# Kernel tuning notes

Measured on AMD Instinct MI355X. Metric: run time of the kernel, lower is better.

Reference implementation:

```python
import jax, jax.numpy as jnp
import numpy as np

C = 1.0            # PoincareBall curvature
BALL_EPS = 4e-3    # geoopt projx eps for float32
MIN_NORM = 1e-15


def artanh(x):
    x = jnp.clip(x, -1.0 + 1e-7, 1.0 - 1e-7)
    return 0.5 * (jnp.log1p(x) - jnp.log1p(-x))


def project(x):
    # geoopt projx: clip norm to (1 - eps) / sqrt(c)
    norm = jnp.maximum(jnp.linalg.norm(x, axis=-1, keepdims=True), MIN_NORM)
    maxnorm = (1.0 - BALL_EPS) / jnp.sqrt(C)
    return jnp.where(norm > maxnorm, x / norm * maxnorm, x)


def mobius_matvec(M, x):
    # geoopt mobius_matvec on PoincareBall (followed by project)
    sqrt_c = jnp.sqrt(C)
    x_norm = jnp.maximum(jnp.linalg.norm(x, axis=-1, keepdims=True), MIN_NORM)
    mx = x @ M.T
    mx_norm = jnp.maximum(jnp.linalg.norm(mx, axis=-1, keepdims=True), MIN_NORM)
    res = jnp.tanh(mx_norm / x_norm * artanh(sqrt_c * x_norm)) * mx / (mx_norm * sqrt_c)
    zero_mx = jnp.all(mx == 0.0, axis=-1, keepdims=True)
    return project(jnp.where(zero_mx, 0.0, res))


def mobius_add(x, y):
    # geoopt mobius_add on PoincareBall (followed by project)
    x2 = jnp.sum(x * x, axis=-1, keepdims=True)
    y2 = jnp.sum(y * y, axis=-1, keepdims=True)
    xy = jnp.sum(x * y, axis=-1, keepdims=True)
    num = (1.0 + 2.0 * C * xy + C * y2) * x + (1.0 - C * x2) * y
    den = jnp.maximum(1.0 + 2.0 * C * xy + C * C * x2 * y2, MIN_NORM)
    return project(num / den)


def hyp_linear(x, W, b):
    out = mobius_matvec(W, x)
    return mobius_add(out, b)


def hyperbolic_scores(q, k):
    # q, k: [B, H, S, Dh]
    eps = 1e-5
    q_norm_sq = jnp.minimum(jnp.sum(q * q, axis=-1, keepdims=True), 1.0 - eps)  # [B,H,S,1]
    k_norm_sq = jnp.minimum(jnp.sum(k * k, axis=-1, keepdims=True), 1.0 - eps)  # [B,H,S,1]
    qk = jnp.einsum('bhqd,bhkd->bhqk', q, k)
    k_norm_sq_t = jnp.swapaxes(k_norm_sq, -2, -1)                               # [B,H,1,S]
    denom = (1.0 - q_norm_sq) * (1.0 - k_norm_sq_t) + eps
    delta = 2.0 * ((qk - q_norm_sq * k_norm_sq_t) / denom)
    dist_sq = jnp.sqrt(jnp.maximum(delta, eps))
    return -dist_sq


def setup_inputs() -> dict:
    key = jax.random.key(0)
    B, S, E = 4, 2048, 512
    ks = jax.random.split(key, 5)
    x = jax.random.normal(ks[0], (B, S, E), dtype=jnp.float32) * 0.02  # inside unit ball
    bound = float(np.sqrt(6.0 / (E + E)))  # xavier_uniform
    def w(k):
        return jax.random.uniform(k, (E, E), dtype=jnp.float32, minval=-bound, maxval=bound)
    z = jnp.zeros((E,), dtype=jnp.float32)
    return {
        'x': x,
        'Wq': w(ks[1]), 'bq': z,
        'Wk': w(ks[2]), 'bk': z,
        'Wv': w(ks[3]), 'bv': z,
        'Wo': w(ks[4]), 'bo': z,
    }


def reference(x, Wq, bq, Wk, bk, Wv, bv, Wo, bo):
    B, S, E = x.shape
    H = 8
    Dh = E // H
    q = hyp_linear(x, Wq, bq)
    k = hyp_linear(x, Wk, bk)
    v = hyp_linear(x, Wv, bv)
    # [B,S,E] -> [B,H,S,Dh]
    split = lambda t: t.reshape(B, S, H, Dh).transpose(0, 2, 1, 3)
    q, k, v = split(q), split(k), split(v)
    scores = hyperbolic_scores(q, k) / jnp.sqrt(jnp.float32(Dh))
    attn = jax.nn.softmax(scores, axis=-1)
    out = jnp.einsum('bhqk,bhkd->bhqd', attn, v)
    out = out.transpose(0, 2, 1, 3).reshape(B, S, E)
    return hyp_linear(out, Wo, bo)
```

## Files before the change

### kernel.cpp

```cpp
#include <hip/hip_runtime.h>
#include <math.h>

#define B_ 4
#define S_ 2048
#define E_ 512
#define H_ 8
#define Dh_ 64
#define BS_ (B_*S_)
#define MAXN 0.996f

typedef __attribute__((ext_vector_type(8))) short short8;
typedef __attribute__((ext_vector_type(4))) float f32x4;

__device__ __forceinline__ unsigned f2bf(float x) {
  unsigned u = __float_as_uint(x);
  return (u + 0x7fffu + ((u >> 16) & 1u)) >> 16;
}
__device__ __forceinline__ float bf2f(unsigned b) {
  return __uint_as_float(b << 16);
}

__device__ __forceinline__ void gload_lds16(const void* g, void* lds) {
  __builtin_amdgcn_global_load_lds(
      (const __attribute__((address_space(1))) unsigned int*)g,
      (__attribute__((address_space(3))) unsigned int*)lds, 16, 0, 0);
}

__global__ __launch_bounds__(256) void pack_w_kernel(const float* __restrict__ W0,
    const float* __restrict__ W1, const float* __restrict__ W2,
    const float* __restrict__ W3, unsigned short* __restrict__ Wp) {
  const float* W = (blockIdx.y == 0) ? W0 : (blockIdx.y == 1) ? W1
                 : (blockIdx.y == 2) ? W2 : W3;
  unsigned short* dst = Wp + (size_t)blockIdx.y * 262144;
  int l = threadIdx.x & 63, tq = threadIdx.x >> 6;
  int n = blockIdx.x;
  int col = 16*n + (l & 15);
  int k0 = 8 * (l >> 4);
  #pragma unroll
  for (int tt = 0; tt < 4; ++tt) {
    int t = tq*4 + tt;
    const float* wp_ = W + (size_t)col * E_ + 32*t + k0;
    float4 a0 = *(const float4*)wp_, a1 = *(const float4*)(wp_ + 4);
    float av[8] = {a0.x,a0.y,a0.z,a0.w,a1.x,a1.y,a1.z,a1.w};
    short8 hi;
    #pragma unroll
    for (int j = 0; j < 8; ++j) hi[j] = (short)f2bf(av[j]);
    *(short8*)(dst + ((size_t)(t*32 + n))*512 + l*8) = hi;
  }
}

__global__ __launch_bounds__(256) void pack_x_kernel(const float* __restrict__ X,
    unsigned short* __restrict__ Xp, float* __restrict__ xn_out,
    float* __restrict__ art_out) {
  __shared__ float sm[4][16];
  int R16 = blockIdx.x;
  int tid = threadIdx.x;
  int wv = tid >> 6, l = tid & 63;
  int l15 = l & 15;
  const float* xrow = X + (size_t)(R16*16 + l15)*E_ + 8*(l >> 4);
  float xsq = 0.f;
  #pragma unroll
  for (int tt = 0; tt < 4; ++tt) {
    int t = wv*4 + tt;
    float4 c0 = *(const float4*)(xrow + 32*t);
    float4 c1 = *(const float4*)(xrow + 32*t + 4);
    float av[8] = {c0.x,c0.y,c0.z,c0.w,c1.x,c1.y,c1.z,c1.w};
    short8 hi, lo;
    #pragma unroll
    for (int j = 0; j < 8; ++j) {
      unsigned hb = f2bf(av[j]);
      hi[j] = (short)hb;
      lo[j] = (short)f2bf(av[j] - bf2f(hb));
      xsq = fmaf(av[j], av[j], xsq);
    }
    unsigned short* o = Xp + ((size_t)(R16*16 + t)*2)*512 + l*8;
    *(short8*)o = hi;
    *(short8*)(o + 512) = lo;
  }
  xsq += __shfl_xor(xsq, 16, 64);
  xsq += __shfl_xor(xsq, 32, 64);
  if (l < 16) sm[wv][l] = xsq;
  __syncthreads();
  if (tid < 16) {
    float s = sm[0][tid] + sm[1][tid] + sm[2][tid] + sm[3][tid];
    float xnv = fmaxf(sqrtf(s), 1e-15f);
    float aa = fminf(xnv, 1.f - 1e-7f);
    xn_out[R16*16 + tid] = xnv;
    art_out[R16*16 + tid] = 0.5f * (log1pf(aa) - log1pf(-aa));
  }
}

__global__ __launch_bounds__(256, 3) void qkv_linear(
    const unsigned short* __restrict__ Xp, const unsigned short* __restrict__ Wp,
    const float* __restrict__ bq_, const float* __restrict__ bk_,
    const float* __restrict__ bv_,
    unsigned short* __restrict__ Qhi, unsigned short* __restrict__ Khi,
    unsigned short* __restrict__ Vhi,
    const float* __restrict__ xn_arr, const float* __restrict__ art_arr,
    float* __restrict__ qn, float* __restrict__ kn) {
  __shared__ float smM[2][4][4][4], smB[2][4][4][4], smb2[4];
  int tid = threadIdx.x;
  int w = tid >> 6, l = tid & 63;
  int l15 = l & 15, g = l >> 4;
  int R = blockIdx.x;
  int mat = blockIdx.y;
  const unsigned short* Wm = Wp + (size_t)mat * 262144;
  const float* bvec = (mat == 0) ? bq_ : (mat == 1) ? bk_ : bv_;
  unsigned short* outHi = (mat == 0) ? Qhi : (mat == 1) ? Khi : Vhi;
  float* normOut = (mat == 0) ? qn : kn;

  f32x4 acc0[8], acc1[8];
  #pragma unroll
  for (int s = 0; s < 8; ++s) {
    acc0[s] = (f32x4){0.f,0.f,0.f,0.f};
    acc1[s] = (f32x4){0.f,0.f,0.f,0.f};
  }
  const unsigned short* xp0 = Xp + ((size_t)(2*R)*16)*1024 + (size_t)l*8;
  const unsigned short* xp1 = Xp + ((size_t)(2*R+1)*16)*1024 + (size_t)l*8;
  const unsigned short* wl = Wm + (size_t)(8*w)*512 + (size_t)l*8;

  #pragma unroll 2
  for (int t = 0; t < 16; ++t) {
    const unsigned short* wb = wl + (size_t)t*16384;
    short8 b[8];
    #pragma unroll
    for (int s = 0; s < 8; ++s) b[s] = *(const short8*)(wb + s*512);
    short8 ahi0 = *(const short8*)(xp0 + t*1024);
    short8 alo0 = *(const short8*)(xp0 + t*1024 + 512);
    short8 ahi1 = *(const short8*)(xp1 + t*1024);
    short8 alo1 = *(const short8*)(xp1 + t*1024 + 512);
    #pragma unroll
    for (int s = 0; s < 8; ++s) {
      acc0[s] = __builtin_amdgcn_mfma_f32_16x16x32_bf16(ahi0, b[s], acc0[s], 0, 0, 0);
      acc0[s] = __builtin_amdgcn_mfma_f32_16x16x32_bf16(alo0, b[s], acc0[s], 0, 0, 0);
      acc1[s] = __builtin_amdgcn_mfma_f32_16x16x32_bf16(ahi1, b[s], acc1[s], 0, 0, 0);
      acc1[s] = __builtin_amdgcn_mfma_f32_16x16x32_bf16(alo1, b[s], acc1[s], 0, 0, 0);
    }
  }

  float xnv4[2][4], art4[2][4];
  #pragma unroll
  for (int rg = 0; rg < 2; ++rg)
    #pragma unroll
    for (int i = 0; i < 4; ++i) {
      int row = R*32 + rg*16 + 4*g + i;
      xnv4[rg][i] = xn_arr[row];
      art4[rg][i] = art_arr[row];
    }

  float bl[8];
  #pragma unroll
  for (int s = 0; s < 8; ++s) bl[s] = bvec[16*(8*w+s) + l15];
  float m2p[2][4] = {{0.f,0.f,0.f,0.f},{0.f,0.f,0.f,0.f}};
  float mbp[2][4] = {{0.f,0.f,0.f,0.f},{0.f,0.f,0.f,0.f}};
  float b2p = 0.f;
  #pragma unroll
  for (int s = 0; s < 8; ++s) {
    b2p += bl[s]*bl[s];
    #pragma unroll
    for (int i = 0; i < 4; ++i) {
      m2p[0][i] = fmaf(acc0[s][i], acc0[s][i], m2p[0][i]);
      mbp[0][i] = fmaf(acc0[s][i], bl[s], mbp[0][i]);
      m2p[1][i] = fmaf(acc1[s][i], acc1[s][i], m2p[1][i]);
      mbp[1][i] = fmaf(acc1[s][i], bl[s], mbp[1][i]);
    }
  }
  #pragma unroll
  for (int off = 1; off <= 8; off <<= 1) {
    b2p += __shfl_xor(b2p, off, 64);
    #pragma unroll
    for (int rg = 0; rg < 2; ++rg)
      #pragma unroll
      for (int i = 0; i < 4; ++i) {
        m2p[rg][i] += __shfl_xor(m2p[rg][i], off, 64);
        mbp[rg][i] += __shfl_xor(mbp[rg][i], off, 64);
      }
  }
  if (l == 0) smb2[w] = b2p;
  if (l15 == 0) {
    #pragma unroll
    for (int rg = 0; rg < 2; ++rg)
      #pragma unroll
      for (int i = 0; i < 4; ++i) { smM[rg][w][g][i] = m2p[rg][i]; smB[rg][w][g][i] = mbp[rg][i]; }
  }
  __syncthreads();
  float b2 = smb2[0] + smb2[1] + smb2[2] + smb2[3];
  float G[2][4], Hc[2][4];
  #pragma unroll
  for (int rg = 0; rg < 2; ++rg)
    #pragma unroll
    for (int i = 0; i < 4; ++i) {
      float m2 = smM[rg][0][g][i]+smM[rg][1][g][i]+smM[rg][2][g][i]+smM[rg][3][g][i];
      float mb = smB[rg][0][g][i]+smB[rg][1][g][i]+smB[rg][2][g][i]+smB[rg][3][g][i];
      float xn = xnv4[rg][i], art = art4[rg][i];
      float mn = fmaxf(sqrtf(m2), 1e-15f);
      float t = tanhf(mn / xn * art);
      float alpha, rn;
      if (m2 > 0.f) { alpha = t / mn; rn = t; } else { alpha = 0.f; rn = 0.f; }
      if (rn > MAXN) { alpha *= MAXN / rn; rn = MAXN; }
      float x2r = rn * rn;
      float xy = alpha * mb;
      float A  = 1.f + 2.f*xy + b2;
      float Bc = 1.f - x2r;
      float den = fmaxf(1.f + 2.f*xy + x2r*b2, 1e-15f);
      float n2v = (A*A*x2r + 2.f*A*Bc*xy + Bc*Bc*b2) / (den*den);
      float nn = fmaxf(sqrtf(n2v), 1e-15f);
      float sc = (nn > MAXN) ? (MAXN / nn) : 1.f;
      G[rg][i]  = sc * A * alpha / den;
      Hc[rg][i] = sc * Bc / den;
    }

  #pragma unroll
  for (int rg = 0; rg < 2; ++rg) {
    const f32x4* acc = rg ? acc1 : acc0;
    #pragma unroll
    for (int i = 0; i < 4; ++i) {
      int grow = R*32 + rg*16 + 4*g + i;
      int bb = grow >> 11, seq = grow & 2047;
      int tile = seq >> 6;
      float hn0 = 0.f, hn1 = 0.f;
      #pragma unroll
      for (int s = 0; s < 8; ++s) {
        int col = 16*(8*w+s) + l15;
        float v = G[rg][i]*acc[s][i] + Hc[rg][i]*bl[s];
        int h = col >> 6, c = col & 63;
        size_t base;
        if (mat == 2) {
          int kt = (seq >> 5) & 1, gp = (seq >> 3) & 3, jv = seq & 7;
          int dn = c >> 4, lt = (c & 15) | (gp << 4);
          base = ((size_t)((bb*8 + h)*32 + tile))*4096 + (size_t)((kt*4+dn)*64 + lt)*8 + jv;
        } else {
          int nf = (seq >> 4) & 3, lt15 = seq & 15;
          int dt = c >> 5, m = (c >> 3) & 3, j = c & 7;
          base = ((size_t)((bb*8 + h)*32 + tile))*4096 + (size_t)((dt*4+nf)*64 + (lt15|(m<<4)))*8 + j;
        }
        outHi[base] = (unsigned short)f2bf(v);
        if (mat < 2) { if (s < 4) hn0 += v*v; else hn1 += v*v; }
      }
      if (mat < 2) {
        hn0 += __shfl_xor(hn0,1,64); hn0 += __shfl_xor(hn0,2,64);
        hn0 += __shfl_xor(hn0,4,64); hn0 += __shfl_xor(hn0,8,64);
        hn1 += __shfl_xor(hn1,1,64); hn1 += __shfl_xor(hn1,2,64);
        hn1 += __shfl_xor(hn1,4,64); hn1 += __shfl_xor(hn1,8,64);
        if (l15 == 0) {
          normOut[((size_t)(bb*8 + 2*w + 0))*S_ + seq] = fminf(hn0, 1.f - 1e-5f);
          normOut[((size_t)(bb*8 + 2*w + 1))*S_ + seq] = fminf(hn1, 1.f - 1e-5f);
        }
      }
    }
  }
}

__global__ __launch_bounds__(256, 3) void o_linear(const float* __restrict__ X,
    const unsigned short* __restrict__ Wp, const float* __restrict__ bvec,
    float* __restrict__ outF) {
  __shared__ float smM[2][4][4][4], smB[2][4][4][4], smb2[4];
  int tid = threadIdx.x;
  int w = tid >> 6, l = tid & 63;
  int l15 = l & 15, g = l >> 4;
  int R = blockIdx.x;

  f32x4 acc0[8], acc1[8];
  #pragma unroll
  for (int s = 0; s < 8; ++s) {
    acc0[s] = (f32x4){0.f,0.f,0.f,0.f};
    acc1[s] = (f32x4){0.f,0.f,0.f,0.f};
  }
  const float* xrow0 = X + (size_t)(R*32 + l15)*E_ + 8*g;
  const float* xrow1 = xrow0 + (size_t)16*E_;
  const unsigned short* wl = Wp + (size_t)(8*w)*512 + (size_t)l*8;

  float4 p00 = *(const float4*)xrow0, p01 = *(const float4*)(xrow0 + 4);
  float4 p10 = *(const float4*)xrow1, p11 = *(const float4*)(xrow1 + 4);
  float xsq0 = 0.f, xsq1 = 0.f;

  #pragma unroll 1
  for (int t = 0; t < 16; ++t) {
    const unsigned short* wb = wl + (size_t)t*16384;
    short8 b[8];
    #pragma unroll
    for (int s = 0; s < 8; ++s) b[s] = *(const short8*)(wb + s*512);
    float a0v[8] = {p00.x,p00.y,p00.z,p00.w,p01.x,p01.y,p01.z,p01.w};
    float a1v[8] = {p10.x,p10.y,p10.z,p10.w,p11.x,p11.y,p11.z,p11.w};
    short8 ahi0, alo0, ahi1, alo1;
    #pragma unroll
    for (int j = 0; j < 8; ++j) {
      unsigned hb0 = f2bf(a0v[j]);
      ahi0[j] = (short)hb0;
      alo0[j] = (short)f2bf(a0v[j] - bf2f(hb0));
      xsq0 = fmaf(a0v[j], a0v[j], xsq0);
      unsigned hb1 = f2bf(a1v[j]);
      ahi1[j] = (short)hb1;
      alo1[j] = (short)f2bf(a1v[j] - bf2f(hb1));
      xsq1 = fmaf(a1v[j], a1v[j], xsq1);
    }
    if (t < 15) {
      p00 = *(const float4*)(xrow0 + 32*(t+1));
      p01 = *(const float4*)(xrow0 + 32*(t+1) + 4);
      p10 = *(const float4*)(xrow1 + 32*(t+1));
      p11 = *(const float4*)(xrow1 + 32*(t+1) + 4);
    }
    #pragma unroll
    for (int s = 0; s < 8; ++s) {
      acc0[s] = __builtin_amdgcn_mfma_f32_16x16x32_bf16(ahi0, b[s], acc0[s], 0, 0, 0);
      acc0[s] = __builtin_amdgcn_mfma_f32_16x16x32_bf16(alo0, b[s], acc0[s], 0, 0, 0);
      acc1[s] = __builtin_amdgcn_mfma_f32_16x16x32_bf16(ahi1, b[s], acc1[s], 0, 0, 0);
      acc1[s] = __builtin_amdgcn_mfma_f32_16x16x32_bf16(alo1, b[s], acc1[s], 0, 0, 0);
    }
  }

  xsq0 += __shfl_xor(xsq0, 16, 64); xsq0 += __shfl_xor(xsq0, 32, 64);
  xsq1 += __shfl_xor(xsq1, 16, 64); xsq1 += __shfl_xor(xsq1, 32, 64);
  float xnv4[2][4], art4[2][4];
  #pragma unroll
  for (int i = 0; i < 4; ++i) {
    float s20 = __shfl(xsq0, 4*g + i, 64);
    float s21 = __shfl(xsq1, 4*g + i, 64);
    float xn0 = fmaxf(sqrtf(s20), 1e-15f);
    float xn1 = fmaxf(sqrtf(s21), 1e-15f);
    float aa0 = fminf(xn0, 1.f - 1e-7f);
    float aa1 = fminf(xn1, 1.f - 1e-7f);
    xnv4[0][i] = xn0; art4[0][i] = 0.5f * (log1pf(aa0) - log1pf(-aa0));
    xnv4[1][i] = xn1; art4[1][i] = 0.5f * (log1pf(aa1) - log1pf(-aa1));
  }

  float bl[8];
  #pragma unroll
  for (int s = 0; s < 8; ++s) bl[s] = bvec[16*(8*w+s) + l15];
  float m2p[2][4] = {{0.f,0.f,0.f,0.f},{0.f,0.f,0.f,0.f}};
  float mbp[2][4] = {{0.f,0.f,0.f,0.f},{0.f,0.f,0.f,0.f}};
  float b2p = 0.f;
  #pragma unroll
  for (int s = 0; s < 8; ++s) {
    b2p += bl[s]*bl[s];
    #pragma unroll
    for (int i = 0; i < 4; ++i) {
      m2p[0][i] = fmaf(acc0[s][i], acc0[s][i], m2p[0][i]);
      mbp[0][i] = fmaf(acc0[s][i], bl[s], mbp[0][i]);
      m2p[1][i] = fmaf(acc1[s][i], acc1[s][i], m2p[1][i]);
      mbp[1][i] = fmaf(acc1[s][i], bl[s], mbp[1][i]);
    }
  }
  #pragma unroll
  for (int off = 1; off <= 8; off <<= 1) {
    b2p += __shfl_xor(b2p, off, 64);
    #pragma unroll
    for (int rg = 0; rg < 2; ++rg)
      #pragma unroll
      for (int i = 0; i < 4; ++i) {
        m2p[rg][i] += __shfl_xor(m2p[rg][i], off, 64);
        mbp[rg][i] += __shfl_xor(mbp[rg][i], off, 64);
      }
  }
  if (l == 0) smb2[w] = b2p;
  if (l15 == 0) {
    #pragma unroll
    for (int rg = 0; rg < 2; ++rg)
      #pragma unroll
      for (int i = 0; i < 4; ++i) { smM[rg][w][g][i] = m2p[rg][i]; smB[rg][w][g][i] = mbp[rg][i]; }
  }
  __syncthreads();
  float b2 = smb2[0] + smb2[1] + smb2[2] + smb2[3];
  #pragma unroll
  for (int rg = 0; rg < 2; ++rg) {
    const f32x4* acc = rg ? acc1 : acc0;
    #pragma unroll
    for (int i = 0; i < 4; ++i) {
      float m2 = smM[rg][0][g][i]+smM[rg][1][g][i]+smM[rg][2][g][i]+smM[rg][3][g][i];
      float mb = smB[rg][0][g][i]+smB[rg][1][g][i]+smB[rg][2][g][i]+smB[rg][3][g][i];
      float xn = xnv4[rg][i], art = art4[rg][i];
      float mn = fmaxf(sqrtf(m2), 1e-15f);
      float t = tanhf(mn / xn * art);
      float alpha, rn;
      if (m2 > 0.f) { alpha = t / mn; rn = t; } else { alpha = 0.f; rn = 0.f; }
      if (rn > MAXN) { alpha *= MAXN / rn; rn = MAXN; }
      float x2r = rn * rn;
      float xy = alpha * mb;
      float A  = 1.f + 2.f*xy + b2;
      float Bc = 1.f - x2r;
      float den = fmaxf(1.f + 2.f*xy + x2r*b2, 1e-15f);
      float n2v = (A*A*x2r + 2.f*A*Bc*xy + Bc*Bc*b2) / (den*den);
      float nn = fmaxf(sqrtf(n2v), 1e-15f);
      float sc = (nn > MAXN) ? (MAXN / nn) : 1.f;
      float Gv = sc * A * alpha / den;
      float Hv = sc * Bc / den;
      int grow = R*32 + rg*16 + 4*g + i;
      #pragma unroll
      for (int s = 0; s < 8; ++s)
        outF[(size_t)grow*E_ + 16*(8*w+s) + l15] = Gv*acc[s][i] + Hv*bl[s];
    }
  }
}

__global__ __launch_bounds__(256, 4) void attn_kernel(
    const unsigned short* __restrict__ Qhi, const unsigned short* __restrict__ Khi,
    const unsigned short* __restrict__ Vhi,
    const float* __restrict__ qn_arr, const float* __restrict__ kn_arr,
    float* __restrict__ Out) {
  __shared__ __align__(16) unsigned short Kf[4096];
  __shared__ __align__(16) unsigned short Vf[2][4096];
  __shared__ __align__(16) unsigned short Pf[4][1024];

  int tid = threadIdx.x;
  int w = tid >> 6, l = tid & 63;
  int l15 = l & 15, g = l >> 4;

  int bid = blockIdx.x;
  int xcd = bid & 7, idx = bid >> 3;
  int bh = xcd * 4 + (idx >> 5);
  int qblk = idx & 31;
  int b = bh >> 3, h = bh & 7;
  int qb = qblk * 64;

  const unsigned short* qbase = Qhi + ((size_t)(bh*32 + qblk))*4096;
  short8 qhi[2];
  #pragma unroll
  for (int dt = 0; dt < 2; ++dt)
    qhi[dt] = *(const short8*)(qbase + (size_t)((dt*4 + w)*64 + l)*8);
  float qnv[4], qd[4], rq[4];
  #pragma unroll
  for (int i = 0; i < 4; ++i) {
    qnv[i] = qn_arr[(size_t)bh*S_ + qb + 16*w + 4*g + i];
    qd[i] = 1.f - qnv[i];
    rq[i] = __builtin_amdgcn_rcpf(qd[i]);
  }

  f32x4 Oacc[4];
  #pragma unroll
  for (int dn = 0; dn < 4; ++dn) Oacc[dn] = (f32x4){0.f,0.f,0.f,0.f};
  float lp[4] = {0.f,0.f,0.f,0.f};

  const unsigned short* Kbh = Khi + ((size_t)bh*32)*4096;
  const unsigned short* Vbh = Vhi + ((size_t)bh*32)*4096;
  const float* knp = kn_arr + (size_t)bh*S_;

  #pragma unroll
  for (int r = 0; r < 2; ++r) {
    gload_lds16(Kbh + r*2048 + w*512 + l*8, &Kf[r*2048 + w*512]);
    gload_lds16(Vbh + r*2048 + w*512 + l*8, &Vf[0][r*2048 + w*512]);
  }
  asm volatile("s_waitcnt vmcnt(0)" ::: "memory");
  __syncthreads();

  #pragma unroll 1
  for (int tile = 0; tile < 32; ++tile) {
    int cur = tile & 1;
    int kb = tile * 64;
    float knc[4];
    #pragma unroll
    for (int n = 0; n < 4; ++n) knc[n] = knp[kb + 16*n + l15];
    #pragma unroll
    for (int n = 0; n < 4; ++n) {
      f32x4 Cn = (f32x4){0.f,0.f,0.f,0.f};
      #pragma unroll
      for (int dt = 0; dt < 2; ++dt) {
        short8 kfr = *(const short8*)&Kf[((dt*4 + n)*64 + l)*8];
        Cn = __builtin_amdgcn_mfma_f32_16x16x32_bf16(qhi[dt], kfr, Cn, 0, 0, 0);
      }
      float kd = 1.f - knc[n];
      float rkn = __builtin_amdgcn_rcpf(kd);
      int cbase = (n >> 1)*64 + 16*((2*n + (l15 >> 3)) & 3) + 4*g;
      int csb = cbase ^ ((cbase >> 3) & 7);
      int j7 = l15 & 7;
      #pragma unroll
      for (int i = 0; i < 4; ++i) {
        float num = fmaf(-qnv[i], knc[n], Cn[i]);
        float d2 = fmaxf(num * (rq[i]*rkn), 5e-6f);
        float sq = d2 * __builtin_amdgcn_rsqf(d2);
        float p = __builtin_amdgcn_exp2f(-0.25503386f * sq);
        unsigned u = __float_as_uint(p);
        lp[i] += __uint_as_float(u & 0xffff0000u);
        Pf[w][((csb ^ i) << 3) + j7] = (unsigned short)(u >> 16);
      }
    }
    __builtin_amdgcn_s_barrier();
    if (tile < 31) {
      const unsigned short* kp = Kbh + ((size_t)(tile+1))*4096;
      const unsigned short* vp = Vbh + ((size_t)(tile+1))*4096;
      #pragma unroll
      for (int r = 0; r < 2; ++r)
        gload_lds16(kp + r*2048 + w*512 + l*8, &Kf[r*2048 + w*512]);
      #pragma unroll
      for (int r = 0; r < 2; ++r)
        gload_lds16(vp + r*2048 + w*512 + l*8, &Vf[cur^1][r*2048 + w*512]);
    }
    __builtin_amdgcn_sched_barrier(0);
    short8 pa0, pa1;
    { int c = l;       int cs = c ^ ((c >> 3) & 7); pa0 = *(const short8*)&Pf[w][cs*8]; }
    { int c = 64 + l;  int cs = c ^ ((c >> 3) & 7); pa1 = *(const short8*)&Pf[w][cs*8]; }
    #pragma unroll
    for (int dn = 0; dn < 4; ++dn) {
      short8 v0 = *(const short8*)&Vf[cur][((0*4 + dn)*64 + l)*8];
      short8 v1 = *(const short8*)&Vf[cur][((1*4 + dn)*64 + l)*8];
      f32x4 o = Oacc[dn];
      o = __builtin_amdgcn_mfma_f32_16x16x32_bf16(pa0, v0, o, 0, 0, 0);
      o = __builtin_amdgcn_mfma_f32_16x16x32_bf16(pa1, v1, o, 0, 0, 0);
      Oacc[dn] = o;
    }
    asm volatile("s_waitcnt vmcnt(2)" ::: "memory");
    __builtin_amdgcn_s_barrier();
  }

  #pragma unroll
  for (int i = 0; i < 4; ++i) {
    lp[i] += __shfl_xor(lp[i], 1, 64);
    lp[i] += __shfl_xor(lp[i], 2, 64);
    lp[i] += __shfl_xor(lp[i], 4, 64);
    lp[i] += __shfl_xor(lp[i], 8, 64);
    lp[i] = 1.f / lp[i];
  }
  #pragma unroll
  for (int i = 0; i < 4; ++i) {
    size_t orow = (size_t)(b*S_ + qb + 16*w + 4*g + i)*E_ + h*Dh_;
    #pragma unroll
    for (int dn = 0; dn < 4; ++dn)
      Out[orow + 16*dn + l15] = Oacc[dn][i] * lp[i];
  }
}

extern "C" void kernel_launch(void* const* d_in, const int* in_sizes, int n_in,
                              void* d_out, int out_size, void* d_ws, size_t ws_size,
                              hipStream_t stream) {
  const float* x  = (const float*)d_in[0];
  const float* Wq = (const float*)d_in[1];
  const float* bq = (const float*)d_in[2];
  const float* Wk = (const float*)d_in[3];
  const float* bk = (const float*)d_in[4];
  const float* Wv = (const float*)d_in[5];
  const float* bv = (const float*)d_in[6];
  const float* Wo = (const float*)d_in[7];
  const float* bo = (const float*)d_in[8];
  float* out = (float*)d_out;

  char* p = (char*)d_ws;
  unsigned short* Wp  = (unsigned short*)p; p += (size_t)2  << 20;
  unsigned short* Xp  = (unsigned short*)p; p += (size_t)17 << 20;
  unsigned short* Qhi = (unsigned short*)p; p += (size_t)8  << 20;
  unsigned short* Khi = (unsigned short*)p; p += (size_t)8  << 20;
  unsigned short* Vhi = (unsigned short*)p; p += (size_t)8  << 20;
  float* ao   = (float*)p; p += (size_t)16 << 20;
  float* xn   = (float*)p; p += BS_ * 4;
  float* art  = (float*)p; p += BS_ * 4;
  float* qn   = (float*)p; p += (size_t)B_*H_*S_ * 4;
  float* kn   = (float*)p; p += (size_t)B_*H_*S_ * 4;

  pack_w_kernel<<<dim3(32, 4), dim3(256), 0, stream>>>(Wq, Wk, Wv, Wo, Wp);
  pack_x_kernel<<<dim3(BS_/16), dim3(256), 0, stream>>>(x, Xp, xn, art);
  qkv_linear<<<dim3(BS_/32, 3), dim3(256), 0, stream>>>(Xp, Wp, bq, bk, bv,
                                                        Qhi, Khi, Vhi, xn, art, qn, kn);
  attn_kernel<<<dim3(1024), dim3(256), 0, stream>>>(Qhi, Khi, Vhi, qn, kn, ao);
  o_linear<<<dim3(BS_/32), dim3(256), 0, stream>>>(ao, Wp + 3*262144, bo, out);
}
```

Before: 160.3 us.

## Double-buffer K tiles in attention and fold key-norm scaling into precomputed rsqrt

K now has two LDS buffers, like V. The next tile's K and V loads are issued at the start of each iteration, which removes the mid-loop barrier that used to separate score computation from the prefetch. The distance scaling is also refactored: instead of a reciprocal of (1-|q|²)(1-|k|²) inside the sqrt, the loop uses a per-row rsqrt for q and a per-key 1/sqrt(1-|k|²). The qkv kernel now precomputes the key term into a new workspace array, which trims per-element ALU work in the inner loop. The trade-offs are more LDS per block, one extra global load per key column, and a slightly different placement of the clamp epsilon.

Measured after the change: 146.0 us. 1.1x faster.

```diff
diff --git a/kernel.cpp b/kernel.cpp
--- a/kernel.cpp
+++ b/kernel.cpp
@@ -97,7 +97,7 @@
     unsigned short* __restrict__ Qhi, unsigned short* __restrict__ Khi,
     unsigned short* __restrict__ Vhi,
     const float* __restrict__ xn_arr, const float* __restrict__ art_arr,
-    float* __restrict__ qn, float* __restrict__ kn) {
+    float* __restrict__ qn, float* __restrict__ kn, float* __restrict__ kni) {
   __shared__ float smM[2][4][4][4], smB[2][4][4][4], smb2[4];
   int tid = threadIdx.x;
   int w = tid >> 6, l = tid & 63;
@@ -243,8 +243,15 @@
         hn1 += __shfl_xor(hn1,1,64); hn1 += __shfl_xor(hn1,2,64);
         hn1 += __shfl_xor(hn1,4,64); hn1 += __shfl_xor(hn1,8,64);
         if (l15 == 0) {
-          normOut[((size_t)(bb*8 + 2*w + 0))*S_ + seq] = fminf(hn0, 1.f - 1e-5f);
-          normOut[((size_t)(bb*8 + 2*w + 1))*S_ + seq] = fminf(hn1, 1.f - 1e-5f);
+          float h0 = fminf(hn0, 1.f - 1e-5f), h1 = fminf(hn1, 1.f - 1e-5f);
+          size_t i0 = ((size_t)(bb*8 + 2*w + 0))*S_ + seq;
+          size_t i1 = ((size_t)(bb*8 + 2*w + 1))*S_ + seq;
+          normOut[i0] = h0;
+          normOut[i1] = h1;
+          if (mat == 1) {
+            kni[i0] = 1.f / sqrtf(1.f - h0);
+            kni[i1] = 1.f / sqrtf(1.f - h1);
+          }
         }
       }
     }
@@ -396,8 +403,8 @@
     const unsigned short* __restrict__ Qhi, const unsigned short* __restrict__ Khi,
     const unsigned short* __restrict__ Vhi,
     const float* __restrict__ qn_arr, const float* __restrict__ kn_arr,
-    float* __restrict__ Out) {
-  __shared__ __align__(16) unsigned short Kf[4096];
+    const float* __restrict__ kni_arr, float* __restrict__ Out) {
+  __shared__ __align__(16) unsigned short Kf[2][4096];
   __shared__ __align__(16) unsigned short Vf[2][4096];
   __shared__ __align__(16) unsigned short Pf[4][1024];
 
@@ -417,12 +424,11 @@
   #pragma unroll
   for (int dt = 0; dt < 2; ++dt)
     qhi[dt] = *(const short8*)(qbase + (size_t)((dt*4 + w)*64 + l)*8);
-  float qnv[4], qd[4], rq[4];
+  float qnv[4], pr[4];
   #pragma unroll
   for (int i = 0; i < 4; ++i) {
     qnv[i] = qn_arr[(size_t)bh*S_ + qb + 16*w + 4*g + i];
-    qd[i] = 1.f - qnv[i];
-    rq[i] = __builtin_amdgcn_rcpf(qd[i]);
+    pr[i] = -0.25503386f * __builtin_amdgcn_rsqf(1.f - qnv[i]);
   }
 
   f32x4 Oacc[4];
@@ -432,11 +438,12 @@
 
   const unsigned short* Kbh = Khi + ((size_t)bh*32)*4096;
   const unsigned short* Vbh = Vhi + ((size_t)bh*32)*4096;
-  const float* knp = kn_arr + (size_t)bh*S_;
+  const float* knp  = kn_arr  + (size_t)bh*S_;
+  const float* knip = kni_arr + (size_t)bh*S_;
 
   #pragma unroll
   for (int r = 0; r < 2; ++r) {
-    gload_lds16(Kbh + r*2048 + w*512 + l*8, &Kf[r*2048 + w*512]);
+    gload_lds16(Kbh + r*2048 + w*512 + l*8, &Kf[0][r*2048 + w*512]);
     gload_lds16(Vbh + r*2048 + w*512 + l*8, &Vf[0][r*2048 + w*512]);
   }
   asm volatile("s_waitcnt vmcnt(0)" ::: "memory");
@@ -446,45 +453,44 @@
   for (int tile = 0; tile < 32; ++tile) {
     int cur = tile & 1;
     int kb = tile * 64;
-    float knc[4];
-    #pragma unroll
-    for (int n = 0; n < 4; ++n) knc[n] = knp[kb + 16*n + l15];
+    float knc[4], kin[4];
+    #pragma unroll
+    for (int n = 0; n < 4; ++n) {
+      knc[n] = knp[kb + 16*n + l15];
+      kin[n] = knip[kb + 16*n + l15];
+    }
+    if (tile < 31) {
+      const unsigned short* kp = Kbh + ((size_t)(tile+1))*4096;
+      const unsigned short* vp = Vbh + ((size_t)(tile+1))*4096;
+      #pragma unroll
+      for (int r = 0; r < 2; ++r) {
+        gload_lds16(kp + r*2048 + w*512 + l*8, &Kf[cur^1][r*2048 + w*512]);
+        gload_lds16(vp + r*2048 + w*512 + l*8, &Vf[cur^1][r*2048 + w*512]);
+      }
+    }
+    __builtin_amdgcn_sched_barrier(0);
     #pragma unroll
     for (int n = 0; n < 4; ++n) {
       f32x4 Cn = (f32x4){0.f,0.f,0.f,0.f};
       #pragma unroll
       for (int dt = 0; dt < 2; ++dt) {
-        short8 kfr = *(const short8*)&Kf[((dt*4 + n)*64 + l)*8];
+        short8 kfr = *(const short8*)&Kf[cur][((dt*4 + n)*64 + l)*8];
         Cn = __builtin_amdgcn_mfma_f32_16x16x32_bf16(qhi[dt], kfr, Cn, 0, 0, 0);
       }
-      float kd = 1.f - knc[n];
-      float rkn = __builtin_amdgcn_rcpf(kd);
       int cbase = (n >> 1)*64 + 16*((2*n + (l15 >> 3)) & 3) + 4*g;
       int csb = cbase ^ ((cbase >> 3) & 7);
       int j7 = l15 & 7;
       #pragma unroll
       for (int i = 0; i < 4; ++i) {
         float num = fmaf(-qnv[i], knc[n], Cn[i]);
-        float d2 = fmaxf(num * (rq[i]*rkn), 5e-6f);
+        float d2 = fmaxf(num, 5e-6f);
         float sq = d2 * __builtin_amdgcn_rsqf(d2);
-        float p = __builtin_amdgcn_exp2f(-0.25503386f * sq);
+        float p = __builtin_amdgcn_exp2f(pr[i] * kin[n] * sq);
         unsigned u = __float_as_uint(p);
         lp[i] += __uint_as_float(u & 0xffff0000u);
         Pf[w][((csb ^ i) << 3) + j7] = (unsigned short)(u >> 16);
       }
     }
-    __builtin_amdgcn_s_barrier();
-    if (tile < 31) {
-      const unsigned short* kp = Kbh + ((size_t)(tile+1))*4096;
-      const unsigned short* vp = Vbh + ((size_t)(tile+1))*4096;
-      #pragma unroll
-      for (int r = 0; r < 2; ++r)
-        gload_lds16(kp + r*2048 + w*512 + l*8, &Kf[r*2048 + w*512]);
-      #pragma unroll
-      for (int r = 0; r < 2; ++r)
-        gload_lds16(vp + r*2048 + w*512 + l*8, &Vf[cur^1][r*2048 + w*512]);
-    }
-    __builtin_amdgcn_sched_barrier(0);
     short8 pa0, pa1;
     { int c = l;       int cs = c ^ ((c >> 3) & 7); pa0 = *(const short8*)&Pf[w][cs*8]; }
     { int c = 64 + l;  int cs = c ^ ((c >> 3) & 7); pa1 = *(const short8*)&Pf[w][cs*8]; }
@@ -497,7 +503,7 @@
       o = __builtin_amdgcn_mfma_f32_16x16x32_bf16(pa1, v1, o, 0, 0, 0);
       Oacc[dn] = o;
     }
-    asm volatile("s_waitcnt vmcnt(2)" ::: "memory");
+    asm volatile("s_waitcnt vmcnt(0)" ::: "memory");
     __builtin_amdgcn_s_barrier();
   }
 
@@ -543,11 +549,12 @@
   float* art  = (float*)p; p += BS_ * 4;
   float* qn   = (float*)p; p += (size_t)B_*H_*S_ * 4;
   float* kn   = (float*)p; p += (size_t)B_*H_*S_ * 4;
+  float* kni  = (float*)p; p += (size_t)B_*H_*S_ * 4;
 
   pack_w_kernel<<<dim3(32, 4), dim3(256), 0, stream>>>(Wq, Wk, Wv, Wo, Wp);
   pack_x_kernel<<<dim3(BS_/16), dim3(256), 0, stream>>>(x, Xp, xn, art);
   qkv_linear<<<dim3(BS_/32, 3), dim3(256), 0, stream>>>(Xp, Wp, bq, bk, bv,
-                                                        Qhi, Khi, Vhi, xn, art, qn, kn);
-  attn_kernel<<<dim3(1024), dim3(256), 0, stream>>>(Qhi, Khi, Vhi, qn, kn, ao);
+                                                        Qhi, Khi, Vhi, xn, art, qn, kn, kni);
+  attn_kernel<<<dim3(1024), dim3(256), 0, stream>>>(Qhi, Khi, Vhi, qn, kn, kni, ao);
   o_linear<<<dim3(BS_/32), dim3(256), 0, stream>>>(ao, Wp + 3*262144, bo, out);
 }
```
